# Kernel tuning notes

Hardware: AMD Instinct MI355X
Metric: run time of the kernel (lower is better)

## Reference

```python
import jax, jax.numpy as jnp
import numpy as np

D, F, E, K = 1024, 2048, 8, 2
EPS = 1.1920929e-07  # torch.finfo(float32).eps, RMSNorm default eps=None


def setup_inputs() -> dict:
    key = jax.random.key(0)
    ks = jax.random.split(key, 6)
    x = jax.random.normal(ks[0], (2, 2048, D), jnp.float32)
    Wg = jax.random.normal(ks[1], (D, E), jnp.float32)          # Gate.weights ~ randn
    norm_w = jnp.ones((E, D), jnp.float32)                       # per-expert RMSNorm weight
    W1 = jax.random.normal(ks[2], (E, D, F), jnp.float32) * 0.02
    b1 = jnp.zeros((E, F), jnp.float32)
    W2 = jax.random.normal(ks[3], (E, D, F), jnp.float32) * 0.02
    b2 = jnp.zeros((E, F), jnp.float32)
    W3 = jax.random.normal(ks[4], (E, F, D), jnp.float32) * 0.02
    b3 = jnp.zeros((E, D), jnp.float32)
    return {"x": x, "Wg": Wg, "norm_w": norm_w, "W1": W1, "b1": b1,
            "W2": W2, "b2": b2, "W3": W3, "b3": b3, "k": K}


def reference(x, Wg, norm_w, W1, b1, W2, b2, W3, b3, k):
    orig_shape = x.shape
    xt = x.reshape(-1, x.shape[-1])                    # [T, d]
    num_experts = Wg.shape[-1]

    # --- Gate: top-k then softmax over selected logits ---
    scores = xt @ Wg                                   # [T, E]
    top_v, top_i = jax.lax.top_k(scores, k)            # [T, k]
    gates = jax.nn.softmax(top_v, axis=-1)             # [T, k]
    # combine weight per (token, expert); zero for unrouted experts
    comb = jnp.einsum('tk,tke->te', gates,
                      jax.nn.one_hot(top_i, num_experts, dtype=gates.dtype))  # [T, E]

    # --- Per-expert SwiGLU FFN with RMSNorm (norm weight folded into W1/W2) ---
    inv = jax.lax.rsqrt(jnp.mean(xt * xt, axis=-1, keepdims=True) + EPS)
    xh = xt * inv                                      # [T, d] (un-weighted RMSNorm)
    W1p = norm_w[:, :, None] * W1                      # [E, d, f]
    W2p = norm_w[:, :, None] * W2
    a = jnp.einsum('td,edf->etf', xh, W1p) + b1[:, None, :]   # [E, T, f]
    g = jnp.einsum('td,edf->etf', xh, W2p) + b2[:, None, :]
    h = jax.nn.silu(a) * g                             # [E, T, f]
    o = jnp.einsum('etf,efd->etd', h, W3) + b3[:, None, :]    # [E, T, d]

    # --- Weighted combine (comb==0 for unrouted -> identical to masked loop) ---
    y = jnp.einsum('etd,te->td', o, comb)              # [T, d]
    return y.reshape(orig_shape)
```

## Files before the change

kernel.cpp:

```cpp
#include <hip/hip_runtime.h>
#include <hip/hip_bf16.h>

typedef unsigned short u16;
typedef __attribute__((ext_vector_type(8))) short bf16x8;
typedef __attribute__((ext_vector_type(4))) float f32x4;

#define D_DIM 1024
#define F_DIM 2048
#define E_NUM 8
#define EPS_RMS 1.1920929e-07f
#define NCHUNK 16

__device__ __forceinline__ u16 f2bf(float f) {
  union { float f; unsigned u; } v; v.f = f;
  unsigned r = v.u + 0x7FFFu + ((v.u >> 16) & 1u);
  return (u16)(r >> 16);
}

__device__ __forceinline__ void async16(const void* g, void* l) {
  __builtin_amdgcn_global_load_lds((const __attribute__((address_space(1))) void*)g,
                                   (__attribute__((address_space(3))) void*)l, 16, 0, 0);
}

__global__ __launch_bounds__(256) void gate_kernel(
    const float* __restrict__ x, const float* __restrict__ Wg,
    u16* __restrict__ xh, int* __restrict__ topi, float* __restrict__ gatev)
{
  const int t = blockIdx.x;
  const int tid = threadIdx.x;
  const float4 xv = reinterpret_cast<const float4*>(x + (size_t)t * D_DIM)[tid];
  float ss = xv.x*xv.x + xv.y*xv.y + xv.z*xv.z + xv.w*xv.w;
  float s[8];
#pragma unroll
  for (int e = 0; e < 8; ++e) s[e] = 0.f;
  const float xa[4] = {xv.x, xv.y, xv.z, xv.w};
#pragma unroll
  for (int j = 0; j < 4; ++j) {
    const float4* wr = reinterpret_cast<const float4*>(Wg + (size_t)(tid*4 + j) * 8);
    float4 w0 = wr[0], w1 = wr[1];
    s[0] += xa[j]*w0.x; s[1] += xa[j]*w0.y; s[2] += xa[j]*w0.z; s[3] += xa[j]*w0.w;
    s[4] += xa[j]*w1.x; s[5] += xa[j]*w1.y; s[6] += xa[j]*w1.z; s[7] += xa[j]*w1.w;
  }
#pragma unroll
  for (int off = 32; off > 0; off >>= 1) {
    ss += __shfl_down(ss, off);
#pragma unroll
    for (int e = 0; e < 8; ++e) s[e] += __shfl_down(s[e], off);
  }
  __shared__ float red[4][9];
  __shared__ float invs;
  const int wv = tid >> 6, lane = tid & 63;
  if (lane == 0) { red[wv][8] = ss;
#pragma unroll
    for (int e = 0; e < 8; ++e) red[wv][e] = s[e]; }
  __syncthreads();
  if (tid == 0) {
    float sum2 = red[0][8] + red[1][8] + red[2][8] + red[3][8];
    invs = rsqrtf(sum2 * (1.0f / D_DIM) + EPS_RMS);
    float sc[8];
#pragma unroll
    for (int e = 0; e < 8; ++e) sc[e] = red[0][e] + red[1][e] + red[2][e] + red[3][e];
    int i0 = 0; float v0 = sc[0];
#pragma unroll
    for (int e = 1; e < 8; ++e) if (sc[e] > v0) { v0 = sc[e]; i0 = e; }
    int i1 = -1; float v1 = -3.0e38f;
#pragma unroll
    for (int e = 0; e < 8; ++e) if (e != i0 && sc[e] > v1) { v1 = sc[e]; i1 = e; }
    float p1 = 1.0f / (1.0f + expf(v0 - v1));
    float p0 = 1.0f - p1;
    topi[2*t] = i0; topi[2*t+1] = i1;
    gatev[2*t] = p0; gatev[2*t+1] = p1;
  }
  __syncthreads();
  const float inv = invs;
  ushort4 o;
  o.x = f2bf(xv.x*inv); o.y = f2bf(xv.y*inv); o.z = f2bf(xv.z*inv); o.w = f2bf(xv.w*inv);
  reinterpret_cast<ushort4*>(xh + (size_t)t * D_DIM)[tid] = o;
}

__global__ __launch_bounds__(256) void count_kernel(
    const int* __restrict__ topi, int* __restrict__ percnt, int nent)
{
  const int blk = blockIdx.x;
  const int tid = threadIdx.x;
  const int per = (nent + NCHUNK*256 - 1) / (NCHUNK*256);
  const int cbase = blk * 256 * per;
  int c[8];
#pragma unroll
  for (int q = 0; q < 8; ++q) c[q] = 0;
  for (int i = 0; i < per; ++i) {
    const int idx = cbase + tid * per + i;
    if (idx < nent) {
      const int e = topi[idx];
#pragma unroll
      for (int q = 0; q < 8; ++q) c[q] += (e == q) ? 1 : 0;
    }
  }
#pragma unroll
  for (int off = 32; off > 0; off >>= 1)
#pragma unroll
    for (int q = 0; q < 8; ++q) c[q] += __shfl_down(c[q], off);
  __shared__ int red[4][8];
  const int wv = tid >> 6, lane = tid & 63;
  if (lane == 0)
#pragma unroll
    for (int q = 0; q < 8; ++q) red[wv][q] = c[q];
  __syncthreads();
  if (tid < 8) percnt[blk * 8 + tid] = red[0][tid] + red[1][tid] + red[2][tid] + red[3][tid];
}

__global__ void scan_kernel(const int* __restrict__ percnt, int* __restrict__ offs,
                            int* __restrict__ base)
{
  if (threadIdx.x == 0) {
    int tot[8];
#pragma unroll
    for (int e = 0; e < 8; ++e) {
      tot[e] = 0;
      for (int c = 0; c < NCHUNK; ++c) tot[e] += percnt[c*8 + e];
    }
    int acc = 0, start[8];
#pragma unroll
    for (int e = 0; e < 8; ++e) { offs[e] = acc; start[e] = acc; acc += (tot[e] + 255) & ~255; }
    offs[8] = acc;
    for (int c = 0; c < NCHUNK; ++c)
#pragma unroll
      for (int e = 0; e < 8; ++e) { base[c*8 + e] = start[e]; start[e] += percnt[c*8 + e]; }
  }
}

__global__ __launch_bounds__(256) void scatter_kernel(
    const int* __restrict__ topi, const int* __restrict__ base,
    int* __restrict__ rowtok, int* __restrict__ slots, int nent)
{
  __shared__ int cur[8];
  const int blk = blockIdx.x, tid = threadIdx.x;
  if (tid < 8) cur[tid] = base[blk*8 + tid];
  __syncthreads();
  const int per = (nent + NCHUNK*256 - 1) / (NCHUNK*256);
  const int cbase = blk * 256 * per;
  for (int i = 0; i < per; ++i) {
    const int idx = cbase + tid * per + i;
    if (idx < nent) {
      const int e = topi[idx];
      const int pos = atomicAdd(&cur[e], 1);
      rowtok[pos] = idx >> 1;
      slots[idx] = pos;
    }
  }
}

__global__ __launch_bounds__(256) void transpose_fold_w12(
    const float* __restrict__ W1, const float* __restrict__ W2,
    const float* __restrict__ scale, u16* __restrict__ Wc)
{
  __shared__ float tile[64][65];
  const int z = blockIdx.z;
  const int e = z & 7;
  const float* W = (z < 8) ? W1 : W2;
  const int gofs = (z < 8) ? 0 : 16;
  const int R = D_DIM, C = F_DIM;
  const int cb = blockIdx.x * 64, rb = blockIdx.y * 64;
  const int tx = threadIdx.x;
  const int ty = threadIdx.y;
  const float* Wp = W + (size_t)e * R * C;
#pragma unroll
  for (int rep = 0; rep < 4; ++rep) {
    const int i = ty + rep * 16;
    float4 v = *reinterpret_cast<const float4*>(Wp + (size_t)(rb + i) * C + cb + tx * 4);
    tile[i][tx*4+0] = v.x; tile[i][tx*4+1] = v.y; tile[i][tx*4+2] = v.z; tile[i][tx*4+3] = v.w;
  }
  __syncthreads();
  float sc[4];
#pragma unroll
  for (int q = 0; q < 4; ++q) sc[q] = scale[(size_t)e * R + rb + tx*4 + q];
  u16* op = Wc + (size_t)e * (2*F_DIM) * D_DIM;
#pragma unroll
  for (int rep = 0; rep < 4; ++rep) {
    const int j = ty + rep * 16;
    const int c = cb + j;
    const int rphys = ((c >> 4) << 5) + (c & 15) + gofs;
    ushort4 o;
    o.x = f2bf(tile[tx*4+0][j] * sc[0]);
    o.y = f2bf(tile[tx*4+1][j] * sc[1]);
    o.z = f2bf(tile[tx*4+2][j] * sc[2]);
    o.w = f2bf(tile[tx*4+3][j] * sc[3]);
    *reinterpret_cast<ushort4*>(op + (size_t)rphys * D_DIM + rb + tx*4) = o;
  }
}

__global__ __launch_bounds__(256) void transpose_w3(
    const float* __restrict__ W, u16* __restrict__ out)
{
  __shared__ float tile[64][65];
  const int e = blockIdx.z;
  const int R = F_DIM, C = D_DIM;
  const int cb = blockIdx.x * 64, rb = blockIdx.y * 64;
  const int tx = threadIdx.x, ty = threadIdx.y;
  const float* Wp = W + (size_t)e * R * C;
#pragma unroll
  for (int rep = 0; rep < 4; ++rep) {
    const int i = ty + rep * 16;
    float4 v = *reinterpret_cast<const float4*>(Wp + (size_t)(rb + i) * C + cb + tx * 4);
    tile[i][tx*4+0] = v.x; tile[i][tx*4+1] = v.y; tile[i][tx*4+2] = v.z; tile[i][tx*4+3] = v.w;
  }
  __syncthreads();
  u16* op = out + (size_t)e * R * C;
#pragma unroll
  for (int rep = 0; rep < 4; ++rep) {
    const int j = ty + rep * 16;
    ushort4 o;
    o.x = f2bf(tile[tx*4+0][j]);
    o.y = f2bf(tile[tx*4+1][j]);
    o.z = f2bf(tile[tx*4+2][j]);
    o.w = f2bf(tile[tx*4+3][j]);
    *reinterpret_cast<ushort4*>(op + (size_t)(cb + j) * R + rb + tx*4) = o;
  }
}

__global__ __launch_bounds__(512, 4) void ffn1_kernel(
    const u16* __restrict__ xh, const u16* __restrict__ Wc,
    const float* __restrict__ b1, const float* __restrict__ b2,
    const int* __restrict__ rowtok, const int* __restrict__ offs,
    u16* __restrict__ h)
{
  __shared__ __align__(16) u16 smem[36864];

  const int row0 = blockIdx.y * 256;
  if (row0 >= offs[8]) return;
  int e = 0;
#pragma unroll
  for (int i = 1; i < 8; ++i) e += (row0 >= offs[i]) ? 1 : 0;

  const int bx = blockIdx.x;
  const int n0p = bx * 128;
  const int tid = threadIdx.x;
  const int lane = tid & 63;
  const int l15 = lane & 15;
  const int wv = tid >> 6;
  const int wm = wv >> 1;
  const int wn = wv & 1;

  int arow[2], aseg[2];
  const u16* gAp[2];
#pragma unroll
  for (int j = 0; j < 2; ++j) {
    const int i = tid + 512*j;
    const int p = i >> 3;
    const int v = (i & 7) ^ (p & 7);
    arow[j] = 2*p + (v >> 2);
    aseg[j] = v & 3;
    int tk = rowtok[row0 + arow[j]];
    if (tk < 0) tk = 0;
    gAp[j] = xh + (size_t)tk * D_DIM + aseg[j] * 8;
  }
  const u16* gBp;
  {
    const int i = tid;
    const int p = i >> 3;
    const int v = (i & 7) ^ (p & 7);
    const int brow = 2*p + (v >> 2);
    gBp = Wc + ((size_t)e * (2*F_DIM) + n0p + brow) * D_DIM + (v & 3) * 8;
  }

  const f32x4 zero = {0.f, 0.f, 0.f, 0.f};
  f32x4 acc[4][4];
#pragma unroll
  for (int i = 0; i < 4; ++i)
#pragma unroll
    for (int j = 0; j < 4; ++j) acc[i][j] = zero;

  const int rlane = (((l15 & 1) << 2) + (lane >> 4)) ^ (l15 >> 1);
  const int aoff = (l15 >> 1) * 64 + rlane * 8;
  const int boff = (l15 >> 1) * 64 + rlane * 8;

#define STAGE1(b, k0)                                                       \
  {                                                                         \
    const int base_ = (b) * 12288;                                          \
    async16(gAp[0] + (k0), &smem[base_ + tid*8]);                           \
    async16(gAp[1] + (k0), &smem[base_ + (tid + 512)*8]);                   \
    async16(gBp   + (k0), &smem[base_ + 8192 + tid*8]);                     \
  }

  STAGE1(0, 0);
  STAGE1(1, 32);

  const int NSTEP = D_DIM / 32;
  for (int t = 0; t < NSTEP; ++t) {
    const int bsel = t % 3;
    if (t + 1 < NSTEP) {
      asm volatile("s_waitcnt vmcnt(3)" ::: "memory");
    } else {
      asm volatile("s_waitcnt vmcnt(0)" ::: "memory");
    }
    __builtin_amdgcn_s_barrier();
    if (t + 2 < NSTEP) {
      const int bn = (t + 2) % 3;
      const int kn = (t + 2) * 32;
      STAGE1(bn, kn);
    }
    const int aB = bsel * 12288, bB = aB + 8192;
    bf16x8 af[4], bv[4];
#pragma unroll
    for (int mi = 0; mi < 4; ++mi)
      af[mi] = *(const bf16x8*)(&smem[aB + (wm*32 + mi*8)*64 + aoff]);
#pragma unroll
    for (int ni = 0; ni < 4; ++ni)
      bv[ni] = *(const bf16x8*)(&smem[bB + (wn*32 + ni*8)*64 + boff]);
#pragma unroll
    for (int mi = 0; mi < 4; ++mi)
#pragma unroll
      for (int ni = 0; ni < 4; ++ni)
        acc[mi][ni] = __builtin_amdgcn_mfma_f32_16x16x32_bf16(af[mi], bv[ni], acc[mi][ni], 0, 0, 0);
  }
#undef STAGE1

#pragma unroll
  for (int mi = 0; mi < 4; ++mi) {
    const int rbase = row0 + wm*64 + mi*16 + (lane >> 4)*4;
#pragma unroll
    for (int q = 0; q < 2; ++q) {
      const int rc = bx*64 + wn*32 + q*16 + l15;
      const float bb1 = b1[e*F_DIM + rc], bb2 = b2[e*F_DIM + rc];
#pragma unroll
      for (int r = 0; r < 4; ++r) {
        float a = acc[mi][2*q][r] + bb1;
        float g = acc[mi][2*q+1][r] + bb2;
        h[(size_t)(rbase + r) * F_DIM + rc] = f2bf(a / (1.f + __expf(-a)) * g);
      }
    }
  }
}

__global__ __launch_bounds__(256, 2) void ffn2_kernel(
    const u16* __restrict__ h, const u16* __restrict__ W3t,
    const float* __restrict__ b3, const int* __restrict__ offs,
    float* __restrict__ opart)
{
  __shared__ __align__(16) u16 smem[32768];

  const int lin = blockIdx.y * gridDim.x + blockIdx.x;
  const int qc  = (gridDim.x * gridDim.y) >> 3;
  const int L   = (lin & 7) * qc + (lin >> 3);
  const int bx  = L % gridDim.x;
  const int by  = L / gridDim.x;

  const int row0 = by * 128;
  if (row0 >= offs[8]) return;
  int e = 0;
#pragma unroll
  for (int i = 1; i < 8; ++i) e += (row0 >= offs[i]) ? 1 : 0;

  const int n0 = bx * 128;
  const int tid = threadIdx.x;
  const int lane = tid & 63;
  const int wv = tid >> 6;
  const int wm = wv >> 1;
  const int wn = wv & 1;

  const int srow = tid >> 3;
  const int sseg = (tid & 7) ^ (srow & 7);
  const u16* gA[4]; const u16* gB[4];
#pragma unroll
  for (int j = 0; j < 4; ++j) {
    gA[j] = h   + (size_t)(row0 + srow + 32*j) * F_DIM + sseg * 8;
    gB[j] = W3t + ((size_t)e * D_DIM + n0 + srow + 32*j) * F_DIM + sseg * 8;
  }

  const f32x4 zero = {0.f, 0.f, 0.f, 0.f};
  f32x4 acc[4][4];
#pragma unroll
  for (int i = 0; i < 4; ++i)
#pragma unroll
    for (int j = 0; j < 4; ++j) acc[i][j] = zero;

  const int rswz = (lane & 7) << 3;
  const int kpart = (lane >> 4) * 8;
  const int arowbase = (wm*64 + (lane & 15)) * 64;
  const int browbase = (wn*64 + (lane & 15)) * 64;

#define STAGE2(b, k0)                                                       \
  {                                                                         \
    const int aB_ = (b)*8192, bB_ = 16384 + (b)*8192;                       \
    _Pragma("unroll")                                                       \
    for (int j = 0; j < 4; ++j) {                                           \
      async16(gA[j] + (k0), &smem[aB_ + (tid + 256*j)*8]);                  \
      async16(gB[j] + (k0), &smem[bB_ + (tid + 256*j)*8]);                  \
    }                                                                       \
  }

  STAGE2(0, 0);
  __syncthreads();

  int cur = 0;
  for (int t = 0; t < F_DIM/64; ++t) {
    if (t + 1 < F_DIM/64) STAGE2(cur ^ 1, (t+1)*64);
    const int aB = cur*8192, bB = 16384 + cur*8192;
#pragma unroll
    for (int kk = 0; kk < 2; ++kk) {
      const int ko = kk*32 + kpart;
      bf16x8 af[4], bv[4];
#pragma unroll
      for (int mi = 0; mi < 4; ++mi)
        af[mi] = *(const bf16x8*)(&smem[aB + ((arowbase + mi*1024 + ko) ^ rswz)]);
#pragma unroll
      for (int ni = 0; ni < 4; ++ni)
        bv[ni] = *(const bf16x8*)(&smem[bB + ((browbase + ni*1024 + ko) ^ rswz)]);
#pragma unroll
      for (int mi = 0; mi < 4; ++mi)
#pragma unroll
        for (int ni = 0; ni < 4; ++ni)
          acc[mi][ni] = __builtin_amdgcn_mfma_f32_16x16x32_bf16(af[mi], bv[ni], acc[mi][ni], 0, 0, 0);
    }
    __syncthreads();
    cur ^= 1;
  }
#undef STAGE2

#pragma unroll
  for (int mi = 0; mi < 4; ++mi) {
    const int rbase = row0 + wm*64 + mi*16 + (lane >> 4)*4;
#pragma unroll
    for (int ni = 0; ni < 4; ++ni) {
      const int gc = n0 + wn*64 + ni*16 + (lane & 15);
      const float bb = b3[e*D_DIM + gc];
#pragma unroll
      for (int r = 0; r < 4; ++r)
        opart[(size_t)(rbase + r) * D_DIM + gc] = acc[mi][ni][r] + bb;
    }
  }
}

__global__ __launch_bounds__(256) void combine_kernel(
    const float* __restrict__ opart, const int* __restrict__ slots,
    const float* __restrict__ gatev, float* __restrict__ y)
{
  const int t = blockIdx.x;
  const int s0 = slots[2*t], s1 = slots[2*t+1];
  const float w0 = gatev[2*t], w1 = gatev[2*t+1];
  const float4 a = reinterpret_cast<const float4*>(opart + (size_t)s0 * D_DIM)[threadIdx.x];
  const float4 b = reinterpret_cast<const float4*>(opart + (size_t)s1 * D_DIM)[threadIdx.x];
  float4 o;
  o.x = w0*a.x + w1*b.x; o.y = w0*a.y + w1*b.y;
  o.z = w0*a.z + w1*b.z; o.w = w0*a.w + w1*b.w;
  reinterpret_cast<float4*>(y + (size_t)t * D_DIM)[threadIdx.x] = o;
}

extern "C" void kernel_launch(void* const* d_in, const int* in_sizes, int n_in,
                              void* d_out, int out_size, void* d_ws, size_t ws_size,
                              hipStream_t stream)
{
  const float* x  = (const float*)d_in[0];
  const float* Wg = (const float*)d_in[1];
  const float* nw = (const float*)d_in[2];
  const float* W1 = (const float*)d_in[3];
  const float* b1 = (const float*)d_in[4];
  const float* W2 = (const float*)d_in[5];
  const float* b2 = (const float*)d_in[6];
  const float* W3 = (const float*)d_in[7];
  const float* b3 = (const float*)d_in[8];
  float* y = (float*)d_out;

  const int T = in_sizes[0] / D_DIM;
  const int NENT = T * 2;
  const int RCAP = ((NENT + E_NUM * 255) + 255) & ~255;
  const int MT1 = RCAP / 256;
  const int MT2 = RCAP / 128;

  char* ws = (char*)d_ws;
  size_t off_ = 0;
  auto take = [&](size_t bytes) { char* p = ws + off_; off_ = (off_ + bytes + 255) & ~(size_t)255; return p; };
  u16* Wc     = (u16*)take((size_t)E_NUM * 2 * F_DIM * D_DIM * 2);
  u16* W3t    = (u16*)take((size_t)E_NUM * D_DIM * F_DIM * 2);
  u16* xh     = (u16*)take((size_t)T * D_DIM * 2);
  u16* hbuf   = (u16*)take((size_t)RCAP * F_DIM * 2);
  int* rowtok = (int*)take((size_t)RCAP * 4);
  int* slots  = (int*)take((size_t)NENT * 4);
  int* topi   = (int*)take((size_t)NENT * 4);
  float* gatev= (float*)take((size_t)NENT * 4);
  int* percnt = (int*)take(NCHUNK * 8 * 4);
  int* cbase  = (int*)take(NCHUNK * 8 * 4);
  int* offs   = (int*)take(64);
  float* opart = (float*)Wc;
  (void)ws_size; (void)n_in; (void)out_size;

  hipMemsetAsync(rowtok, 0xFF, (size_t)RCAP * 4, stream);

  transpose_fold_w12<<<dim3(F_DIM/64, D_DIM/64, 2*E_NUM), dim3(16, 16), 0, stream>>>(W1, W2, nw, Wc);
  transpose_w3<<<dim3(D_DIM/64, F_DIM/64, E_NUM), dim3(16, 16), 0, stream>>>(W3, W3t);

  gate_kernel<<<T, 256, 0, stream>>>(x, Wg, xh, topi, gatev);
  count_kernel<<<NCHUNK, 256, 0, stream>>>(topi, percnt, NENT);
  scan_kernel<<<1, 64, 0, stream>>>(percnt, offs, cbase);
  scatter_kernel<<<NCHUNK, 256, 0, stream>>>(topi, cbase, rowtok, slots, NENT);

  ffn1_kernel<<<dim3(F_DIM/64, MT1), 512, 0, stream>>>(xh, Wc, b1, b2, rowtok, offs, hbuf);
  ffn2_kernel<<<dim3(D_DIM/128, MT2), 256, 0, stream>>>(hbuf, W3t, b3, offs, opart);
  combine_kernel<<<T, 256, 0, stream>>>(opart, slots, gatev, y);
}
```

Measured before the change: 241.5 us.

## Enlarge ffn1 tile to 256x256 and interleave async prefetch with MFMA phases

The ffn1 GEMM block tile grows from 256 rows by 128 interleaved W1/W2 columns to 256 by 256, with 8 waves arranged 2x4 so each wave owns a 128x64 accumulator tile. The aim is more operand reuse per LDS load and fewer blocks re-reading the gathered activations. Next-stage global-to-LDS prefetches are split into four pieces and issued between MFMA phases to spread memory traffic across the compute. In exchange, accumulator registers double and LDS use grows, so occupancy is lowered to 2 blocks per CU and the grid has half as many column blocks.

```diff
diff --git a/kernel.cpp b/kernel.cpp
--- a/kernel.cpp
+++ b/kernel.cpp
@@ -218,13 +218,13 @@
   }
 }
 
-__global__ __launch_bounds__(512, 4) void ffn1_kernel(
+__global__ __launch_bounds__(512, 2) void ffn1_kernel(
     const u16* __restrict__ xh, const u16* __restrict__ Wc,
     const float* __restrict__ b1, const float* __restrict__ b2,
     const int* __restrict__ rowtok, const int* __restrict__ offs,
     u16* __restrict__ h)
 {
-  __shared__ __align__(16) u16 smem[36864];
+  __shared__ __align__(16) u16 smem[49152];
 
   const int row0 = blockIdx.y * 256;
   if (row0 >= offs[8]) return;
@@ -232,100 +232,98 @@
 #pragma unroll
   for (int i = 1; i < 8; ++i) e += (row0 >= offs[i]) ? 1 : 0;
 
-  const int bx = blockIdx.x;
-  const int n0p = bx * 128;
+  const int n0p = blockIdx.x * 256;
   const int tid = threadIdx.x;
   const int lane = tid & 63;
   const int l15 = lane & 15;
   const int wv = tid >> 6;
-  const int wm = wv >> 1;
-  const int wn = wv & 1;
-
-  int arow[2], aseg[2];
-  const u16* gAp[2];
+  const int wm = wv >> 2;
+  const int wn = wv & 3;
+
+  const u16* gAp[2]; const u16* gBp[2];
 #pragma unroll
   for (int j = 0; j < 2; ++j) {
     const int i = tid + 512*j;
     const int p = i >> 3;
     const int v = (i & 7) ^ (p & 7);
-    arow[j] = 2*p + (v >> 2);
-    aseg[j] = v & 3;
-    int tk = rowtok[row0 + arow[j]];
+    const int row = 2*p + (v >> 2);
+    const int seg = v & 3;
+    int tk = rowtok[row0 + row];
     if (tk < 0) tk = 0;
-    gAp[j] = xh + (size_t)tk * D_DIM + aseg[j] * 8;
-  }
-  const u16* gBp;
-  {
-    const int i = tid;
-    const int p = i >> 3;
-    const int v = (i & 7) ^ (p & 7);
-    const int brow = 2*p + (v >> 2);
-    gBp = Wc + ((size_t)e * (2*F_DIM) + n0p + brow) * D_DIM + (v & 3) * 8;
+    gAp[j] = xh + (size_t)tk * D_DIM + seg * 8;
+    gBp[j] = Wc + ((size_t)e * (2*F_DIM) + n0p + row) * D_DIM + seg * 8;
   }
 
   const f32x4 zero = {0.f, 0.f, 0.f, 0.f};
-  f32x4 acc[4][4];
-#pragma unroll
-  for (int i = 0; i < 4; ++i)
+  f32x4 acc[8][4];
+#pragma unroll
+  for (int i = 0; i < 8; ++i)
 #pragma unroll
     for (int j = 0; j < 4; ++j) acc[i][j] = zero;
 
   const int rlane = (((l15 & 1) << 2) + (lane >> 4)) ^ (l15 >> 1);
-  const int aoff = (l15 >> 1) * 64 + rlane * 8;
-  const int boff = (l15 >> 1) * 64 + rlane * 8;
-
-#define STAGE1(b, k0)                                                       \
-  {                                                                         \
-    const int base_ = (b) * 12288;                                          \
-    async16(gAp[0] + (k0), &smem[base_ + tid*8]);                           \
-    async16(gAp[1] + (k0), &smem[base_ + (tid + 512)*8]);                   \
-    async16(gBp   + (k0), &smem[base_ + 8192 + tid*8]);                     \
-  }
-
-  STAGE1(0, 0);
-  STAGE1(1, 32);
+  const int roff = (l15 >> 1) * 64 + rlane * 8;
+
+#define ST_A(b, k0, j) async16(gAp[j] + (k0), &smem[(b)*16384 + (tid + 512*(j))*8]);
+#define ST_B(b, k0, j) async16(gBp[j] + (k0), &smem[(b)*16384 + 8192 + (tid + 512*(j))*8]);
+
+  ST_A(0, 0, 0)  ST_A(0, 0, 1)  ST_B(0, 0, 0)  ST_B(0, 0, 1)
+  ST_A(1, 32, 0) ST_A(1, 32, 1) ST_B(1, 32, 0) ST_B(1, 32, 1)
 
   const int NSTEP = D_DIM / 32;
   for (int t = 0; t < NSTEP; ++t) {
-    const int bsel = t % 3;
     if (t + 1 < NSTEP) {
-      asm volatile("s_waitcnt vmcnt(3)" ::: "memory");
+      asm volatile("s_waitcnt vmcnt(4)" ::: "memory");
     } else {
       asm volatile("s_waitcnt vmcnt(0)" ::: "memory");
     }
     __builtin_amdgcn_s_barrier();
-    if (t + 2 < NSTEP) {
-      const int bn = (t + 2) % 3;
-      const int kn = (t + 2) * 32;
-      STAGE1(bn, kn);
-    }
-    const int aB = bsel * 12288, bB = aB + 8192;
-    bf16x8 af[4], bv[4];
-#pragma unroll
-    for (int mi = 0; mi < 4; ++mi)
-      af[mi] = *(const bf16x8*)(&smem[aB + (wm*32 + mi*8)*64 + aoff]);
-#pragma unroll
-    for (int ni = 0; ni < 4; ++ni)
-      bv[ni] = *(const bf16x8*)(&smem[bB + (wn*32 + ni*8)*64 + boff]);
-#pragma unroll
-    for (int mi = 0; mi < 4; ++mi)
-#pragma unroll
-      for (int ni = 0; ni < 4; ++ni)
-        acc[mi][ni] = __builtin_amdgcn_mfma_f32_16x16x32_bf16(af[mi], bv[ni], acc[mi][ni], 0, 0, 0);
-  }
-#undef STAGE1
-
-#pragma unroll
-  for (int mi = 0; mi < 4; ++mi) {
-    const int rbase = row0 + wm*64 + mi*16 + (lane >> 4)*4;
+    const int aB = (t % 3) * 16384, bB = aB + 8192;
+    const int bn = (t + 2) % 3;
+    const int kn = (t + 2) * 32;
+    const bool pf = (t + 2 < NSTEP);
+
+    bf16x8 bv[4];
+#pragma unroll
+    for (int ct = 0; ct < 4; ++ct)
+      bv[ct] = *(const bf16x8*)(&smem[bB + (wn*32 + ct*8)*64 + roff]);
+
+#pragma unroll
+    for (int ph = 0; ph < 4; ++ph) {
+      if (pf) {
+        if (ph == 0)      { ST_A(bn, kn, 0) }
+        else if (ph == 1) { ST_A(bn, kn, 1) }
+        else if (ph == 2) { ST_B(bn, kn, 0) }
+        else              { ST_B(bn, kn, 1) }
+      }
+      bf16x8 af[2];
+#pragma unroll
+      for (int j = 0; j < 2; ++j) {
+        const int rt = ph*2 + j;
+        af[j] = *(const bf16x8*)(&smem[aB + (wm*64 + rt*8)*64 + roff]);
+      }
+#pragma unroll
+      for (int j = 0; j < 2; ++j)
+#pragma unroll
+        for (int ct = 0; ct < 4; ++ct)
+          acc[ph*2 + j][ct] = __builtin_amdgcn_mfma_f32_16x16x32_bf16(af[j], bv[ct], acc[ph*2 + j][ct], 0, 0, 0);
+    }
+  }
+#undef ST_A
+#undef ST_B
+
+  const int rcbase = (n0p + wn*64) >> 1;
+#pragma unroll
+  for (int rt = 0; rt < 8; ++rt) {
+    const int rbase = row0 + wm*128 + rt*16 + (lane >> 4)*4;
 #pragma unroll
     for (int q = 0; q < 2; ++q) {
-      const int rc = bx*64 + wn*32 + q*16 + l15;
+      const int rc = rcbase + q*16 + l15;
       const float bb1 = b1[e*F_DIM + rc], bb2 = b2[e*F_DIM + rc];
 #pragma unroll
       for (int r = 0; r < 4; ++r) {
-        float a = acc[mi][2*q][r] + bb1;
-        float g = acc[mi][2*q+1][r] + bb2;
+        float a = acc[rt][2*q][r] + bb1;
+        float g = acc[rt][2*q+1][r] + bb2;
         h[(size_t)(rbase + r) * F_DIM + rc] = f2bf(a / (1.f + __expf(-a)) * g);
       }
     }
@@ -494,7 +492,7 @@
   scan_kernel<<<1, 64, 0, stream>>>(percnt, offs, cbase);
   scatter_kernel<<<NCHUNK, 256, 0, stream>>>(topi, cbase, rowtok, slots, NENT);
 
-  ffn1_kernel<<<dim3(F_DIM/64, MT1), 512, 0, stream>>>(xh, Wc, b1, b2, rowtok, offs, hbuf);
+  ffn1_kernel<<<dim3((2*F_DIM)/256, MT1), 512, 0, stream>>>(xh, Wc, b1, b2, rowtok, offs, hbuf);
   ffn2_kernel<<<dim3(D_DIM/128, MT2), 256, 0, stream>>>(hbuf, W3t, b3, offs, opart);
   combine_kernel<<<T, 256, 0, stream>>>(opart, slots, gatev, y);
 }
```

After: 248.2 us. 2.8% more time.
